# Kernel tuning notes

Measured on AMD Instinct MI355X. Metric: run time of the kernel, lower is better.

## Reference

```python
import jax, jax.numpy as jnp
import numpy as np
import math

HEAD_DIM = 64
RP_DIM = 256
B, H, N = 4, 8, 4096
EPS = 1e-4  # performer positive-feature epsilon


def _ortho_gaussian_matrix(m, d, seed=0):
    # gaussian_orthogonal_random_matrix, scaling=0: stack QR-orthogonalized
    # d x d gaussian blocks, scale rows by norms of an iid gaussian matrix.
    rng = np.random.default_rng(seed)
    blocks = []
    for _ in range(int(np.ceil(m / d))):
        g = rng.standard_normal((d, d))
        q, _ = np.linalg.qr(g)
        blocks.append(q.T)
    mat = np.concatenate(blocks, axis=0)[:m]
    multiplier = np.linalg.norm(rng.standard_normal((m, d)), axis=1)
    return (multiplier[:, None] * mat).astype(np.float32)


def _softmax_features(x, proj, is_query):
    # FAVOR+ positive random features: ratio * exp(Wx - ||x||^2/2 - stab) + eps
    ratio = proj.shape[0] ** -0.5
    xp = jnp.einsum('bhnd,md->bhnm', x, proj)
    diag = 0.5 * jnp.sum(x * x, axis=-1, keepdims=True)
    if is_query:
        stab = jnp.max(xp, axis=-1, keepdims=True)
    else:
        stab = jnp.max(xp, axis=(-1, -2), keepdims=True)
    return ratio * (jnp.exp(xp - diag - stab) + EPS)


def setup_inputs() -> dict:
    key = jax.random.key(0)
    kq, kk, kv = jax.random.split(key, 3)
    Q = jax.random.normal(kq, (B, H, N, HEAD_DIM), dtype=jnp.float32)
    K = jax.random.normal(kk, (B, H, N, HEAD_DIM), dtype=jnp.float32)
    V = jax.random.normal(kv, (B, H, N, HEAD_DIM), dtype=jnp.float32)
    mask = jnp.ones((B, N), dtype=jnp.float32)
    projection = jnp.asarray(_ortho_gaussian_matrix(RP_DIM, HEAD_DIM, seed=0))
    return {'Q': Q, 'K': K, 'V': V, 'mask': mask, 'projection': projection}


def reference(Q, K, V, mask, projection):
    scale = HEAD_DIM ** -0.25  # 1/sqrt(sqrt(head_dim))
    m = mask[:, None, :, None]
    q = Q * scale
    k = K * scale * m
    v = V * m
    phi_q = _softmax_features(q, projection, is_query=True)   # [b,h,n,m]
    phi_k = _softmax_features(k, projection, is_query=False)  # [b,h,n,m]
    # non-causal linear attention
    k_sum = jnp.sum(phi_k, axis=2)                                   # [b,h,m]
    D_inv = 1.0 / jnp.einsum('bhnm,bhm->bhn', phi_q, k_sum)          # [b,h,n]
    context = jnp.einsum('bhnm,bhne->bhme', phi_k, v)                # [b,h,m,e]
    out = jnp.einsum('bhme,bhnm,bhn->bhne', context, phi_q, D_inv)   # [b,h,n,e]
    return out
```

## Files before the change

### kernel.cpp

```cpp
#include <hip/hip_runtime.h>
#include <hip/hip_bf16.h>


typedef __attribute__((ext_vector_type(8))) short short8;
typedef __attribute__((ext_vector_type(4))) float floatx4;

constexpr int BB = 4, HH = 8, NN = 4096, DD = 64, MM = 256, BH = 32;
constexpr int NCH = 16;
constexpr float SCALE = 0.3535533905932738f;
constexpr float RATIO = 0.0625f;
constexpr float EPSI  = 1e-4f;
constexpr float NEGINF = -3.4e38f;

__device__ inline unsigned pk2(float a, float b) {
  unsigned ua = __float_as_uint(a) + 0x8000u;
  unsigned ub = __float_as_uint(b) + 0x8000u;
  return (ua >> 16) | (ub & 0xffff0000u);
}
__device__ inline float hif(float x) {
  return __uint_as_float((__float_as_uint(x) + 0x8000u) & 0xffff0000u);
}
__device__ inline unsigned short bhi(float x) {
  return (unsigned short)((__float_as_uint(x) + 0x8000u) >> 16);
}
__device__ inline int ph16(int i) { return (i & 56) | ((i + (i >> 3)) & 7); }

union Frag { short8 s8; unsigned u[4]; };

__device__ inline void atomicMaxF(float* a, float v) {
  unsigned* ai = (unsigned*)a;
  unsigned old = __atomic_load_n(ai, __ATOMIC_RELAXED);
  while (__uint_as_float(old) < v) {
    unsigned assumed = old;
    old = atomicCAS(ai, assumed, __float_as_uint(v));
    if (old == assumed) break;
  }
}

__global__ __launch_bounds__(256) void prep_kernel(
    const float* __restrict__ proj, unsigned short* __restrict__ projH,
    unsigned short* __restrict__ projL, float* __restrict__ stabk,
    float* __restrict__ Vs, float* __restrict__ ctxsum,
    float* __restrict__ ksE) {
  const int i = blockIdx.x * 256 + threadIdx.x;
  float v = proj[i];
  projH[i] = bhi(v);
  projL[i] = bhi(v - hif(v));
  if (i < BH) stabk[i] = NEGINF;
  if (i < 2048) { Vs[i] = 0.f; ctxsum[i] = 0.f; }
  if (i < 8192) ksE[i] = 0.f;
}

template <bool PARTIAL>
__global__ __launch_bounds__(256) void kside_kernel(
    const float* __restrict__ K, const float* __restrict__ V,
    const float* __restrict__ mask,
    const unsigned short* __restrict__ projH, const unsigned short* __restrict__ projL,
    float* __restrict__ stabk, float* __restrict__ ksE,
    float* __restrict__ ctxOut, float* __restrict__ Vs) {
  const int bh = blockIdx.y, b = bh >> 3;
  const int t = threadIdx.x;
  const int w = t >> 6, l = t & 63, c = l & 15, sq = l >> 4;
  const int m0 = w * 64;

  __shared__ __align__(16) unsigned short sK[2][32 * 72];
  __shared__ __align__(16) unsigned short sVt[2][64 * 40];
  __shared__ float sDiag[32];
  __shared__ float sRed[4];
  __shared__ float sVsum[4][64];
  __shared__ __align__(16) unsigned short sPhi[4][2][512];

  Frag Bp[4][2][2];
#pragma unroll
  for (int tt = 0; tt < 4; ++tt)
#pragma unroll
    for (int s = 0; s < 2; ++s) {
      const size_t o = (size_t)(m0 + tt * 16 + c) * DD + s * 32 + sq * 8;
      Bp[tt][s][0].s8 = *(const short8*)&projH[o];
      Bp[tt][s][1].s8 = *(const short8*)&projL[o];
    }

  floatx4 ctxacc[4][4];
#pragma unroll
  for (int i = 0; i < 4; ++i)
#pragma unroll
    for (int j = 0; j < 4; ++j) ctxacc[i][j] = (floatx4){0.f, 0.f, 0.f, 0.f};
  float ksac[4] = {0.f, 0.f, 0.f, 0.f};
  float mxloc = NEGINF;
  float vsacc = 0.f;

  const int r0 = blockIdx.x * 256;

  float4 pk4[2], pv4[2];
  float pmk[2], pmv[2];
  {
    const int rb = r0;
#pragma unroll
    for (int rep = 0; rep < 2; ++rep) {
      const int f = t + rep * 256;
      const int n = f >> 4;
      pmk[rep] = mask[b * NN + rb + n];
      pk4[rep] = *(const float4*)(K + ((size_t)bh * NN + rb + n) * DD + (f & 15) * 4);
      const int n_loc = w * 4 + rep * 16 + sq;
      pmv[rep] = mask[b * NN + rb + n_loc];
      pv4[rep] = *(const float4*)(V + ((size_t)bh * NN + rb + n_loc) * DD + c * 4);
    }
  }

  for (int ch = 0; ch < 8; ++ch) {
    __syncthreads();

#pragma unroll
    for (int rep = 0; rep < 2; ++rep) {
      const int f = t + rep * 256;
      const int n = f >> 4, dg = f & 15;
      const float msc = pmk[rep] * SCALE;
      float k0 = pk4[rep].x * msc, k1 = pk4[rep].y * msc,
            k2 = pk4[rep].z * msc, k3 = pk4[rep].w * msc;
      float ss = fmaf(k0, k0, fmaf(k1, k1, fmaf(k2, k2, k3 * k3)));
      ss += __shfl_xor(ss, 1); ss += __shfl_xor(ss, 2);
      ss += __shfl_xor(ss, 4); ss += __shfl_xor(ss, 8);
      if (dg == 0) sDiag[n] = 0.5f * ss;
      unsigned h0 = pk2(k0, k1), h1 = pk2(k2, k3);
      float q0 = k0 - hif(k0), q1 = k1 - hif(k1);
      float q2 = k2 - hif(k2), q3 = k3 - hif(k3);
      *(uint2*)(&sK[0][n * 72 + dg * 4]) = make_uint2(h0, h1);
      *(uint2*)(&sK[1][n * 72 + dg * 4]) = make_uint2(pk2(q0, q1), pk2(q2, q3));
    }

#pragma unroll
    for (int rep = 0; rep < 2; ++rep) {
      const int nb = w * 4 + rep * 16;
      const float mk = pmv[rep];
      float4 vv = pv4[rep];
      float va[4] = {vv.x * mk, vv.y * mk, vv.z * mk, vv.w * mk};
      float g[4];
#pragma unroll
      for (int k = 0; k < 4; ++k) {
        const int gi = (sq + k) & 3;
        float sel = va[(sq - k) & 3];
        g[gi] = __shfl(sel, gi * 16 + c);
      }
      const int estar = c * 4 + sq;
      vsacc += ((g[0] + g[1]) + (g[2] + g[3]));
      unsigned h0 = pk2(g[0], g[1]), h1 = pk2(g[2], g[3]);
      float q0 = g[0] - hif(g[0]), q1 = g[1] - hif(g[1]);
      float q2 = g[2] - hif(g[2]), q3 = g[3] - hif(g[3]);
      *(uint2*)(&sVt[0][estar * 40 + nb]) = make_uint2(h0, h1);
      *(uint2*)(&sVt[1][estar * 40 + nb]) = make_uint2(pk2(q0, q1), pk2(q2, q3));
    }
    __syncthreads();

    if (ch < 7) {
      const int rb = r0 + (ch + 1) * 32;
#pragma unroll
      for (int rep = 0; rep < 2; ++rep) {
        const int f = t + rep * 256;
        const int n = f >> 4;
        pmk[rep] = mask[b * NN + rb + n];
        pk4[rep] = *(const float4*)(K + ((size_t)bh * NN + rb + n) * DD + (f & 15) * 4);
        const int n_loc = w * 4 + rep * 16 + sq;
        pmv[rep] = mask[b * NN + rb + n_loc];
        pv4[rep] = *(const float4*)(V + ((size_t)bh * NN + rb + n_loc) * DD + c * 4);
      }
    }

    Frag Ak[2][2][2];
#pragma unroll
    for (int i = 0; i < 2; ++i)
#pragma unroll
      for (int s = 0; s < 2; ++s) {
        Ak[i][s][0].s8 = *(const short8*)&sK[0][(i * 16 + c) * 72 + s * 32 + sq * 8];
        Ak[i][s][1].s8 = *(const short8*)&sK[1][(i * 16 + c) * 72 + s * 32 + sq * 8];
      }
    Frag Bv[4][2];
#pragma unroll
    for (int E = 0; E < 4; ++E) {
      Bv[E][0].s8 = *(const short8*)&sVt[0][(E * 16 + c) * 40 + sq * 8];
      Bv[E][1].s8 = *(const short8*)&sVt[1][(E * 16 + c) * 40 + sq * 8];
    }

    __builtin_amdgcn_s_setprio(1);
#pragma unroll
    for (int tt = 0; tt < 4; ++tt) {
      floatx4 xacc[2];
#pragma unroll
      for (int i = 0; i < 2; ++i) {
        floatx4 a = (floatx4){0.f, 0.f, 0.f, 0.f};
#pragma unroll
        for (int s = 0; s < 2; ++s) {
          a = __builtin_amdgcn_mfma_f32_16x16x32_bf16(Ak[i][s][0].s8, Bp[tt][s][0].s8, a, 0, 0, 0);
          a = __builtin_amdgcn_mfma_f32_16x16x32_bf16(Ak[i][s][0].s8, Bp[tt][s][1].s8, a, 0, 0, 0);
          a = __builtin_amdgcn_mfma_f32_16x16x32_bf16(Ak[i][s][1].s8, Bp[tt][s][0].s8, a, 0, 0, 0);
        }
        xacc[i] = a;
      }
      const int qp_c = sq >> 1, half = (sq & 1) * 4;
#pragma unroll
      for (int i = 0; i < 2; ++i) {
        float p[4];
#pragma unroll
        for (int jj = 0; jj < 4; ++jj) {
          float xp = xacc[i][jj];
          mxloc = fmaxf(mxloc, xp);
          p[jj] = __expf(xp - sDiag[i * 16 + sq * 4 + jj]);
          ksac[tt] += p[jj];
        }
        unsigned h0 = pk2(p[0], p[1]), h1 = pk2(p[2], p[3]);
        float q0 = p[0] - hif(p[0]), q1 = p[1] - hif(p[1]);
        float q2 = p[2] - hif(p[2]), q3 = p[3] - hif(p[3]);
        const int tl = (i * 2 + qp_c) * 16 + c;
        const int idx = ph16(tl) * 8 + half;
        *(uint2*)&sPhi[w][0][idx] = make_uint2(h0, h1);
        *(uint2*)&sPhi[w][1][idx] = make_uint2(pk2(q0, q1), pk2(q2, q3));
      }
      Frag Ap[2];
      Ap[0].s8 = *(const short8*)&sPhi[w][0][ph16(l) * 8];
      Ap[1].s8 = *(const short8*)&sPhi[w][1][ph16(l) * 8];
#pragma unroll
      for (int E = 0; E < 4; ++E) {
        ctxacc[tt][E] = __builtin_amdgcn_mfma_f32_16x16x32_bf16(Ap[0].s8, Bv[E][0].s8, ctxacc[tt][E], 0, 0, 0);
        ctxacc[tt][E] = __builtin_amdgcn_mfma_f32_16x16x32_bf16(Ap[0].s8, Bv[E][1].s8, ctxacc[tt][E], 0, 0, 0);
        ctxacc[tt][E] = __builtin_amdgcn_mfma_f32_16x16x32_bf16(Ap[1].s8, Bv[E][0].s8, ctxacc[tt][E], 0, 0, 0);
      }
    }
    __builtin_amdgcn_s_setprio(0);
  }

#pragma unroll
  for (int tt = 0; tt < 4; ++tt) {
    float v = ksac[tt];
    v += __shfl_xor(v, 16);
    v += __shfl_xor(v, 32);
    if (sq == 0) atomicAdd(&ksE[bh * MM + m0 + tt * 16 + c], v);
  }
#pragma unroll
  for (int off = 1; off <= 32; off <<= 1) mxloc = fmaxf(mxloc, __shfl_xor(mxloc, off));
  if (l == 0) sRed[w] = mxloc;
  sVsum[w][c * 4 + sq] = vsacc;
  __syncthreads();
  if (t == 0)
    atomicMaxF(&stabk[bh], fmaxf(fmaxf(sRed[0], sRed[1]), fmaxf(sRed[2], sRed[3])));
  if (t < 64)
    atomicAdd(&Vs[bh * DD + t],
              (sVsum[0][t] + sVsum[1][t]) + (sVsum[2][t] + sVsum[3][t]));

  if (PARTIAL) {
    float* cg = ctxOut + ((size_t)(bh * NCH + blockIdx.x) * MM) * DD;
#pragma unroll
    for (int tt = 0; tt < 4; ++tt)
#pragma unroll
      for (int E = 0; E < 4; ++E)
#pragma unroll
        for (int r = 0; r < 4; ++r)
          cg[(m0 + tt * 16 + sq * 4 + r) * DD + E * 16 + c] = ctxacc[tt][E][r];
  } else {
    float* cg = ctxOut + (size_t)bh * MM * DD;
#pragma unroll
    for (int tt = 0; tt < 4; ++tt)
#pragma unroll
      for (int E = 0; E < 4; ++E)
#pragma unroll
        for (int r = 0; r < 4; ++r)
          atomicAdd(&cg[(m0 + tt * 16 + sq * 4 + r) * DD + E * 16 + c],
                    ctxacc[tt][E][r]);
  }
}

template <int NPARTS>
__global__ __launch_bounds__(256) void fixup_kernel(
    const float* __restrict__ stabk, const float* __restrict__ Vs,
    const float* __restrict__ ksE, const float* __restrict__ ctxParts,
    float* __restrict__ ksum, float* __restrict__ kssum,
    float* __restrict__ ctxsum, unsigned short* __restrict__ ctxTH,
    unsigned short* __restrict__ ctxTL) {
  const int bh = blockIdx.y, mc = blockIdx.x, t = threadIdx.x;
  const float es = __expf(-stabk[bh]);
  const int e = t & 63, g = t >> 6;
  const float vse = EPSI * Vs[bh * DD + e];

  __shared__ float tile[64 * 33];
  __shared__ float cred[256];

  float csum = 0.f;
#pragma unroll
  for (int r = 0; r < 8; ++r) {
    const int ml = r * 4 + g;
    const int m = mc * 32 + ml;
    float x = 0.f;
#pragma unroll
    for (int p = 0; p < NPARTS; ++p)
      x += ctxParts[(((size_t)bh * NPARTS + p) * MM + m) * DD + e];
    float v = RATIO * (es * x + vse);
    csum += v;
    tile[e * 33 + ml] = v;
  }
  cred[t] = csum;
  __syncthreads();
  if (t < 64)
    atomicAdd(&ctxsum[bh * DD + t],
              (cred[t] + cred[t + 64]) + (cred[t + 128] + cred[t + 192]));

  {
    const int ml5 = t & 31, elg = t >> 5;
#pragma unroll
    for (int r = 0; r < 8; ++r) {
      const int el = r * 8 + elg;
      float v = tile[el * 33 + ml5];
      const size_t o = ((size_t)(bh * DD + el)) * MM + mc * 32 + ml5;
      ctxTH[o] = bhi(v);
      ctxTL[o] = bhi(v - hif(v));
    }
  }

  if (mc == 0) {
    __syncthreads();
    const float kv = RATIO * (es * ksE[bh * MM + t] + (float)NN * EPSI);
    ksum[bh * MM + t] = kv;
    cred[t] = kv;
    __syncthreads();
    for (int off = 128; off >= 1; off >>= 1) {
      if (t < off) cred[t] += cred[t + off];
      __syncthreads();
    }
    if (t == 0) kssum[bh] = cred[0];
  }
}

__global__ __launch_bounds__(256, 2) void out_kernel(
    const float* __restrict__ Q,
    const unsigned short* __restrict__ projH, const unsigned short* __restrict__ projL,
    const float* __restrict__ ksum,
    const unsigned short* __restrict__ ctxTH, const unsigned short* __restrict__ ctxTL,
    const float* __restrict__ kssum, const float* __restrict__ ctxsum,
    float* __restrict__ out) {
  const int bh = blockIdx.y;
  const int r0 = blockIdx.x * 64;
  const int t = threadIdx.x, w = t >> 6, l = t & 63, c = l & 15, sq = l >> 4;

  __shared__ __align__(16) unsigned short sQ[2][64 * 80];
  __shared__ __align__(16) unsigned short sP[2][64 * 80];
  __shared__ __align__(16) unsigned short sC[2][64 * 80];
  __shared__ float sKs[256];
  __shared__ float sDiag[64];
  __shared__ __align__(16) unsigned short sPhi[4][2][2][512];

  {
    const int row = t >> 2, q4 = t & 3;
    const float* qp = Q + ((size_t)bh * NN + r0 + row) * DD + q4 * 16;
    float4 t0 = *(const float4*)(qp + 0), t1 = *(const float4*)(qp + 4),
           t2 = *(const float4*)(qp + 8), t3 = *(const float4*)(qp + 12);
    float v[16] = {t0.x, t0.y, t0.z, t0.w, t1.x, t1.y, t1.z, t1.w,
                   t2.x, t2.y, t2.z, t2.w, t3.x, t3.y, t3.z, t3.w};
    float ss = 0.f;
#pragma unroll
    for (int j = 0; j < 16; ++j) { v[j] *= SCALE; ss = fmaf(v[j], v[j], ss); }
    ss += __shfl_xor(ss, 1);
    ss += __shfl_xor(ss, 2);
    if (q4 == 0) sDiag[row] = 0.5f * ss;
    unsigned short* dh = &sQ[0][row * 80 + q4 * 16];
    unsigned short* dl = &sQ[1][row * 80 + q4 * 16];
#pragma unroll
    for (int j = 0; j < 8; ++j) {
      *(unsigned*)&dh[2 * j] = pk2(v[2 * j], v[2 * j + 1]);
      float l0 = v[2 * j] - hif(v[2 * j]), l1 = v[2 * j + 1] - hif(v[2 * j + 1]);
      *(unsigned*)&dl[2 * j] = pk2(l0, l1);
    }
  }
  sKs[t] = ksum[bh * MM + t];
  __syncthreads();

  Frag Bq[2][2];
#pragma unroll
  for (int s = 0; s < 2; ++s)
#pragma unroll
    for (int p = 0; p < 2; ++p)
      Bq[s][p].s8 = *(const short8*)&sQ[p][(w * 16 + c) * 80 + s * 32 + sq * 8];

  const float diagc = sDiag[w * 16 + c];
  floatx4 oacc[4];
#pragma unroll
  for (int E = 0; E < 4; ++E) oacc[E] = (floatx4){0.f, 0.f, 0.f, 0.f};
  float mxacc = NEGINF, dsacc = 0.f;

  for (int mc = 0; mc < 4; ++mc) {
    __syncthreads();
    {
      const int row = t >> 2, q4 = t & 3;
      const size_t gp = (size_t)(mc * 64 + row) * DD + q4 * 16;
      const uint4* ph = (const uint4*)&projH[gp];
      const uint4* pl = (const uint4*)&projL[gp];
      *(uint4*)&sP[0][row * 80 + q4 * 16] = ph[0];
      *(uint4*)&sP[0][row * 80 + q4 * 16 + 8] = ph[1];
      *(uint4*)&sP[1][row * 80 + q4 * 16] = pl[0];
      *(uint4*)&sP[1][row * 80 + q4 * 16 + 8] = pl[1];
      const size_t gc = ((size_t)bh * DD + row) * MM + mc * 64 + q4 * 16;
      const uint4* chh = (const uint4*)&ctxTH[gc];
      const uint4* cll = (const uint4*)&ctxTL[gc];
      *(uint4*)&sC[0][row * 80 + q4 * 16] = chh[0];
      *(uint4*)&sC[0][row * 80 + q4 * 16 + 8] = chh[1];
      *(uint4*)&sC[1][row * 80 + q4 * 16] = cll[0];
      *(uint4*)&sC[1][row * 80 + q4 * 16 + 8] = cll[1];
    }
    __syncthreads();

    __builtin_amdgcn_s_setprio(1);
#pragma unroll
    for (int tt = 0; tt < 4; ++tt) {
      Frag Af[2][2];
#pragma unroll
      for (int s = 0; s < 2; ++s)
#pragma unroll
        for (int p = 0; p < 2; ++p)
          Af[s][p].s8 = *(const short8*)&sP[p][(tt * 16 + c) * 80 + s * 32 + sq * 8];
      floatx4 x = (floatx4){0.f, 0.f, 0.f, 0.f};
#pragma unroll
      for (int s = 0; s < 2; ++s) {
        x = __builtin_amdgcn_mfma_f32_16x16x32_bf16(Af[s][0].s8, Bq[s][0].s8, x, 0, 0, 0);
        x = __builtin_amdgcn_mfma_f32_16x16x32_bf16(Af[s][0].s8, Bq[s][1].s8, x, 0, 0, 0);
        x = __builtin_amdgcn_mfma_f32_16x16x32_bf16(Af[s][1].s8, Bq[s][0].s8, x, 0, 0, 0);
      }
      float p4[4];
#pragma unroll
      for (int jj = 0; jj < 4; ++jj) {
        const float xp = x[jj];
        mxacc = fmaxf(mxacc, xp);
        p4[jj] = __expf(xp - diagc);
        dsacc = fmaf(p4[jj], sKs[mc * 64 + tt * 16 + sq * 4 + jj], dsacc);
      }
      const int kstep = tt >> 1;
      const int tl = ((tt & 1) * 2 + (sq >> 1)) * 16 + c;
      const int off = (sq & 1) * 4;
      float l0 = p4[0] - hif(p4[0]), l1 = p4[1] - hif(p4[1]);
      float l2 = p4[2] - hif(p4[2]), l3 = p4[3] - hif(p4[3]);
      *(uint2*)&sPhi[w][0][kstep][tl * 8 + off] = make_uint2(pk2(p4[0], p4[1]), pk2(p4[2], p4[3]));
      *(uint2*)&sPhi[w][1][kstep][tl * 8 + off] = make_uint2(pk2(l0, l1), pk2(l2, l3));
    }

#pragma unroll
    for (int ks = 0; ks < 2; ++ks) {
      Frag Aph[2];
      Aph[0].s8 = *(const short8*)&sPhi[w][0][ks][l * 8];
      Aph[1].s8 = *(const short8*)&sPhi[w][1][ks][l * 8];
#pragma unroll
      for (int E = 0; E < 4; ++E) {
        Frag Bc0, Bc1;
        Bc0.s8 = *(const short8*)&sC[0][(E * 16 + c) * 80 + ks * 32 + sq * 8];
        Bc1.s8 = *(const short8*)&sC[1][(E * 16 + c) * 80 + ks * 32 + sq * 8];
        oacc[E] = __builtin_amdgcn_mfma_f32_16x16x32_bf16(Aph[0].s8, Bc0.s8, oacc[E], 0, 0, 0);
        oacc[E] = __builtin_amdgcn_mfma_f32_16x16x32_bf16(Aph[0].s8, Bc1.s8, oacc[E], 0, 0, 0);
        oacc[E] = __builtin_amdgcn_mfma_f32_16x16x32_bf16(Aph[1].s8, Bc0.s8, oacc[E], 0, 0, 0);
      }
    }
    __builtin_amdgcn_s_setprio(0);
  }

  mxacc = fmaxf(mxacc, __shfl_xor(mxacc, 16));
  mxacc = fmaxf(mxacc, __shfl_xor(mxacc, 32));
  dsacc += __shfl_xor(dsacc, 16);
  dsacc += __shfl_xor(dsacc, 32);

  const float kss = kssum[bh];
  float fac[4], oinv[4];
#pragma unroll
  for (int jj = 0; jj < 4; ++jj) {
    const int src = sq * 4 + jj;
    const float s_row = __shfl(mxacc, src);
    const float d_row = __shfl(dsacc, src);
    const float f = __expf(s_row) * EPSI;
    fac[jj] = f;
    oinv[jj] = 1.f / (d_row + f * kss);
  }

  const float* csb = ctxsum + bh * DD;
#pragma unroll
  for (int E = 0; E < 4; ++E) {
    const float cse = csb[E * 16 + c];
#pragma unroll
    for (int jj = 0; jj < 4; ++jj) {
      const int row = r0 + w * 16 + sq * 4 + jj;
      out[((size_t)bh * NN + row) * DD + E * 16 + c] =
          (oacc[E][jj] + fac[jj] * cse) * oinv[jj];
    }
  }
}

extern "C" void kernel_launch(void* const* d_in, const int* in_sizes, int n_in,
                              void* d_out, int out_size, void* d_ws, size_t ws_size,
                              hipStream_t stream) {
  const float* Q    = (const float*)d_in[0];
  const float* K    = (const float*)d_in[1];
  const float* V    = (const float*)d_in[2];
  const float* mask = (const float*)d_in[3];
  const float* proj = (const float*)d_in[4];
  float* out = (float*)d_out;

  float* wsf = (float*)d_ws;
  float* stabk  = wsf;
  float* ksum   = wsf + 32;
  float* kssum  = wsf + 8224;
  float* Vs     = wsf + 8256;
  float* ctxsum = wsf + 10304;
  float* ksE    = wsf + 12352;
  unsigned short* projH = (unsigned short*)(wsf + 20544);
  unsigned short* projL = (unsigned short*)(wsf + 28736);
  unsigned short* ctxTH = (unsigned short*)(wsf + 36928);
  unsigned short* ctxTL = (unsigned short*)(wsf + 299072);
  float* ctxBig = wsf + 561216;

  const size_t need_partial = (size_t)(561216 + NCH * BH * MM * DD) * 4;
  const bool partial = ws_size >= need_partial;

  prep_kernel<<<64, 256, 0, stream>>>(proj, projH, projL, stabk, Vs, ctxsum, ksE);

  if (partial) {
    kside_kernel<true><<<dim3(NCH, BH), 256, 0, stream>>>(
        K, V, mask, projH, projL, stabk, ksE, ctxBig, Vs);
    fixup_kernel<NCH><<<dim3(8, BH), 256, 0, stream>>>(
        stabk, Vs, ksE, ctxBig, ksum, kssum, ctxsum, ctxTH, ctxTL);
  } else {
    hipMemsetAsync(ctxBig, 0, (size_t)MM * DD * BH * 4, stream);
    kside_kernel<false><<<dim3(NCH, BH), 256, 0, stream>>>(
        K, V, mask, projH, projL, stabk, ksE, ctxBig, Vs);
    fixup_kernel<1><<<dim3(8, BH), 256, 0, stream>>>(
        stabk, Vs, ksE, ctxBig, ksum, kssum, ctxsum, ctxTH, ctxTL);
  }

  out_kernel<<<dim3(64, BH), 256, 0, stream>>>(
      Q, projH, projL, ksum, ctxTH, ctxTL, kssum, ctxsum, out);
}
```

Before: 225.5 us.

## Stage whole projection and context in LDS once, build Q fragments in registers

The output kernel now loads the full projection (256x64 hi/lo) and the per-head transposed context (64x256 hi/lo) into shared memory once at the start. This replaces four per-chunk reloads, each bracketed by two block barriers. Q is read directly in MFMA fragment layout and split into bf16 hi/lo in registers, which removes the sQ/sDiag staging and a shared-memory round trip. LDS use rises to roughly 140 KB, so the launch-bounds occupancy hint is dropped and fewer blocks can be resident per CU, leaving less latency hiding.

```diff
diff --git a/kernel.cpp b/kernel.cpp
--- a/kernel.cpp
+++ b/kernel.cpp
@@ -327,7 +327,7 @@
   }
 }
 
-__global__ __launch_bounds__(256, 2) void out_kernel(
+__global__ __launch_bounds__(256) void out_kernel(
     const float* __restrict__ Q,
     const unsigned short* __restrict__ projH, const unsigned short* __restrict__ projL,
     const float* __restrict__ ksum,
@@ -338,81 +338,79 @@
   const int r0 = blockIdx.x * 64;
   const int t = threadIdx.x, w = t >> 6, l = t & 63, c = l & 15, sq = l >> 4;
 
-  __shared__ __align__(16) unsigned short sQ[2][64 * 80];
-  __shared__ __align__(16) unsigned short sP[2][64 * 80];
-  __shared__ __align__(16) unsigned short sC[2][64 * 80];
+  __shared__ __align__(16) unsigned short sP[2][256 * 72];
+  __shared__ __align__(16) unsigned short sC[2][64 * 264];
+  __shared__ __align__(16) unsigned short sPhi[4][2][2][512];
   __shared__ float sKs[256];
-  __shared__ float sDiag[64];
-  __shared__ __align__(16) unsigned short sPhi[4][2][2][512];
-
+
+  const unsigned short* ctxH_b = ctxTH + (size_t)bh * DD * MM;
+  const unsigned short* ctxL_b = ctxTL + (size_t)bh * DD * MM;
+
+#pragma unroll
+  for (int seg = 0; seg < 8; ++seg) {
+    const int gch = seg * 256 + t;
+    const int prow = gch >> 3, j = gch & 7;
+    *(uint4*)&sP[0][prow * 72 + j * 8] =
+        *(const uint4*)&projH[(size_t)prow * DD + j * 8];
+    *(uint4*)&sP[1][prow * 72 + j * 8] =
+        *(const uint4*)&projL[(size_t)prow * DD + j * 8];
+  }
+#pragma unroll
+  for (int seg = 0; seg < 8; ++seg) {
+    const int gch = seg * 256 + t;
+    const int e = gch >> 5, jm = gch & 31;
+    *(uint4*)&sC[0][e * 264 + jm * 8] =
+        *(const uint4*)&ctxH_b[(size_t)e * MM + jm * 8];
+    *(uint4*)&sC[1][e * 264 + jm * 8] =
+        *(const uint4*)&ctxL_b[(size_t)e * MM + jm * 8];
+  }
+  sKs[t] = ksum[bh * MM + t];
+
+  Frag Bq[2][2];
+  float diagc;
   {
-    const int row = t >> 2, q4 = t & 3;
-    const float* qp = Q + ((size_t)bh * NN + r0 + row) * DD + q4 * 16;
-    float4 t0 = *(const float4*)(qp + 0), t1 = *(const float4*)(qp + 4),
-           t2 = *(const float4*)(qp + 8), t3 = *(const float4*)(qp + 12);
-    float v[16] = {t0.x, t0.y, t0.z, t0.w, t1.x, t1.y, t1.z, t1.w,
-                   t2.x, t2.y, t2.z, t2.w, t3.x, t3.y, t3.z, t3.w};
+    const float* qrow = Q + ((size_t)bh * NN + r0 + w * 16 + c) * DD;
+    float v[16];
     float ss = 0.f;
 #pragma unroll
+    for (int s = 0; s < 2; ++s) {
+      float4 a0 = *(const float4*)(qrow + s * 32 + sq * 8);
+      float4 a1 = *(const float4*)(qrow + s * 32 + sq * 8 + 4);
+      v[s * 8 + 0] = a0.x; v[s * 8 + 1] = a0.y; v[s * 8 + 2] = a0.z; v[s * 8 + 3] = a0.w;
+      v[s * 8 + 4] = a1.x; v[s * 8 + 5] = a1.y; v[s * 8 + 6] = a1.z; v[s * 8 + 7] = a1.w;
+    }
+#pragma unroll
     for (int j = 0; j < 16; ++j) { v[j] *= SCALE; ss = fmaf(v[j], v[j], ss); }
-    ss += __shfl_xor(ss, 1);
-    ss += __shfl_xor(ss, 2);
-    if (q4 == 0) sDiag[row] = 0.5f * ss;
-    unsigned short* dh = &sQ[0][row * 80 + q4 * 16];
-    unsigned short* dl = &sQ[1][row * 80 + q4 * 16];
-#pragma unroll
-    for (int j = 0; j < 8; ++j) {
-      *(unsigned*)&dh[2 * j] = pk2(v[2 * j], v[2 * j + 1]);
-      float l0 = v[2 * j] - hif(v[2 * j]), l1 = v[2 * j + 1] - hif(v[2 * j + 1]);
-      *(unsigned*)&dl[2 * j] = pk2(l0, l1);
-    }
-  }
-  sKs[t] = ksum[bh * MM + t];
+    ss += __shfl_xor(ss, 16);
+    ss += __shfl_xor(ss, 32);
+    diagc = 0.5f * ss;
+#pragma unroll
+    for (int s = 0; s < 2; ++s)
+#pragma unroll
+      for (int k = 0; k < 4; ++k) {
+        float a = v[s * 8 + 2 * k], b2 = v[s * 8 + 2 * k + 1];
+        Bq[s][0].u[k] = pk2(a, b2);
+        Bq[s][1].u[k] = pk2(a - hif(a), b2 - hif(b2));
+      }
+  }
   __syncthreads();
 
-  Frag Bq[2][2];
-#pragma unroll
-  for (int s = 0; s < 2; ++s)
-#pragma unroll
-    for (int p = 0; p < 2; ++p)
-      Bq[s][p].s8 = *(const short8*)&sQ[p][(w * 16 + c) * 80 + s * 32 + sq * 8];
-
-  const float diagc = sDiag[w * 16 + c];
   floatx4 oacc[4];
 #pragma unroll
   for (int E = 0; E < 4; ++E) oacc[E] = (floatx4){0.f, 0.f, 0.f, 0.f};
   float mxacc = NEGINF, dsacc = 0.f;
 
+#pragma unroll
   for (int mc = 0; mc < 4; ++mc) {
-    __syncthreads();
-    {
-      const int row = t >> 2, q4 = t & 3;
-      const size_t gp = (size_t)(mc * 64 + row) * DD + q4 * 16;
-      const uint4* ph = (const uint4*)&projH[gp];
-      const uint4* pl = (const uint4*)&projL[gp];
-      *(uint4*)&sP[0][row * 80 + q4 * 16] = ph[0];
-      *(uint4*)&sP[0][row * 80 + q4 * 16 + 8] = ph[1];
-      *(uint4*)&sP[1][row * 80 + q4 * 16] = pl[0];
-      *(uint4*)&sP[1][row * 80 + q4 * 16 + 8] = pl[1];
-      const size_t gc = ((size_t)bh * DD + row) * MM + mc * 64 + q4 * 16;
-      const uint4* chh = (const uint4*)&ctxTH[gc];
-      const uint4* cll = (const uint4*)&ctxTL[gc];
-      *(uint4*)&sC[0][row * 80 + q4 * 16] = chh[0];
-      *(uint4*)&sC[0][row * 80 + q4 * 16 + 8] = chh[1];
-      *(uint4*)&sC[1][row * 80 + q4 * 16] = cll[0];
-      *(uint4*)&sC[1][row * 80 + q4 * 16 + 8] = cll[1];
-    }
-    __syncthreads();
-
-    __builtin_amdgcn_s_setprio(1);
 #pragma unroll
     for (int tt = 0; tt < 4; ++tt) {
       Frag Af[2][2];
 #pragma unroll
-      for (int s = 0; s < 2; ++s)
-#pragma unroll
-        for (int p = 0; p < 2; ++p)
-          Af[s][p].s8 = *(const short8*)&sP[p][(tt * 16 + c) * 80 + s * 32 + sq * 8];
+      for (int s = 0; s < 2; ++s) {
+        const int a = (mc * 64 + tt * 16 + c) * 72 + s * 32 + sq * 8;
+        Af[s][0].s8 = *(const short8*)&sP[0][a];
+        Af[s][1].s8 = *(const short8*)&sP[1][a];
+      }
       floatx4 x = (floatx4){0.f, 0.f, 0.f, 0.f};
 #pragma unroll
       for (int s = 0; s < 2; ++s) {
@@ -444,15 +442,15 @@
       Aph[1].s8 = *(const short8*)&sPhi[w][1][ks][l * 8];
 #pragma unroll
       for (int E = 0; E < 4; ++E) {
+        const int a = (E * 16 + c) * 264 + mc * 64 + ks * 32 + sq * 8;
         Frag Bc0, Bc1;
-        Bc0.s8 = *(const short8*)&sC[0][(E * 16 + c) * 80 + ks * 32 + sq * 8];
-        Bc1.s8 = *(const short8*)&sC[1][(E * 16 + c) * 80 + ks * 32 + sq * 8];
+        Bc0.s8 = *(const short8*)&sC[0][a];
+        Bc1.s8 = *(const short8*)&sC[1][a];
         oacc[E] = __builtin_amdgcn_mfma_f32_16x16x32_bf16(Aph[0].s8, Bc0.s8, oacc[E], 0, 0, 0);
         oacc[E] = __builtin_amdgcn_mfma_f32_16x16x32_bf16(Aph[0].s8, Bc1.s8, oacc[E], 0, 0, 0);
         oacc[E] = __builtin_amdgcn_mfma_f32_16x16x32_bf16(Aph[1].s8, Bc0.s8, oacc[E], 0, 0, 0);
       }
     }
-    __builtin_amdgcn_s_setprio(0);
   }
 
   mxacc = fmaxf(mxacc, __shfl_xor(mxacc, 16));
@@ -478,8 +476,8 @@
     const float cse = csb[E * 16 + c];
 #pragma unroll
     for (int jj = 0; jj < 4; ++jj) {
-      const int row = r0 + w * 16 + sq * 4 + jj;
-      out[((size_t)bh * NN + row) * DD + E * 16 + c] =
+      const int row2 = r0 + w * 16 + sq * 4 + jj;
+      out[((size_t)bh * NN + row2) * DD + E * 16 + c] =
           (oacc[E][jj] + fac[jj] * cse) * oinv[jj];
     }
   }
```

Result: slower. 239.4 us (+6.2%).
